# Performance work log

Measured on AMD Instinct MI355X. Metric: run time of the kernel, lower is better.

Reference implementation:

```python
import jax, jax.numpy as jnp
import numpy as np

B, N, S, K = 8, 4096, 2048, 64          # clouds, points/cloud, fps samples (ratio=0.5), max neighbors
C_IN, HID, OUT = 64, 128, 128
RADIUS = 0.2
EPS = 1e-5


def fps(p, s):
    """Farthest point sampling on p:[N,3]; deterministic start at index 0. Returns [s] indices."""
    def step(carry, _):
        min_d, last = carry
        d = jnp.sum((p - p[last]) ** 2, axis=-1)
        min_d = jnp.minimum(min_d, d)
        return (min_d, jnp.argmax(min_d).astype(jnp.int32)), last
    init = (jnp.full((p.shape[0],), jnp.inf, p.dtype), jnp.int32(0))
    _, idx = jax.lax.scan(step, init, None, length=s)
    return idx


def bn_act(h, g, be, mask):
    # masked batch-norm over all valid edges (training-mode stats), then ReLU
    m = mask[..., None].astype(h.dtype)
    cnt = jnp.sum(m)
    mean = jnp.sum(h * m, axis=(0, 1, 2)) / cnt
    var = jnp.sum(((h - mean) ** 2) * m, axis=(0, 1, 2)) / cnt
    return jax.nn.relu((h - mean) * jax.lax.rsqrt(var + EPS) * g + be)


def setup_inputs() -> dict:
    key = jax.random.key(0)
    ks = jax.random.split(key, 8)
    x = jax.random.normal(ks[0], (B * N, C_IN), jnp.float32)
    pos = jax.random.uniform(ks[1], (B * N, 3), jnp.float32)
    batch = jnp.repeat(jnp.arange(B, dtype=jnp.int32), N)
    c0 = C_IN + 3
    W0 = jax.random.normal(ks[2], (c0, HID), jnp.float32) / np.sqrt(c0).astype(np.float32)
    W1 = jax.random.normal(ks[3], (HID, HID), jnp.float32) / np.sqrt(HID).astype(np.float32)
    W2 = jax.random.normal(ks[4], (HID, OUT), jnp.float32) / np.sqrt(HID).astype(np.float32)
    z = lambda n: jnp.zeros((n,), jnp.float32)
    o = lambda n: jnp.ones((n,), jnp.float32)
    return dict(x=x, pos=pos, batch=batch,
                W0=W0, b0=z(HID), g0=o(HID), be0=z(HID),
                W1=W1, b1=z(HID), g1=o(HID), be1=z(HID),
                W2=W2, b2=z(OUT))


def reference(x, pos, batch, W0, b0, g0, be0, W1, b1, g1, be1, W2, b2):
    posb = pos.reshape(B, N, 3)
    xb = x.reshape(B, N, C_IN)
    idx = jax.vmap(lambda p: fps(p, S))(posb)                       # [B,S]
    ctr = jnp.take_along_axis(posb, idx[..., None], axis=1)          # [B,S,3] sampled centroids
    # radius graph: K nearest within RADIUS (mask the rest)
    d2 = jnp.sum((ctr[:, :, None, :] - posb[:, None, :, :]) ** 2, axis=-1)  # [B,S,N]
    negd, nbr = jax.lax.top_k(-d2, K)                                # [B,S,K]
    mask = (-negd) <= RADIUS ** 2
    bix = jnp.arange(B)[:, None, None]
    pos_j = posb[bix, nbr]                                           # [B,S,K,3]
    x_j = xb[bix, nbr]                                               # [B,S,K,C_IN]
    feat = jnp.concatenate([x_j, pos_j - ctr[:, :, None, :]], axis=-1)  # [B,S,K,C_IN+3]
    h = bn_act(feat @ W0 + b0, g0, be0, mask)
    h = bn_act(h @ W1 + b1, g1, be1, mask)
    h = h @ W2 + b2                                                  # plain last layer
    h = jnp.where(mask[..., None], h, -jnp.inf)
    out = jnp.max(h, axis=2)                                         # max aggregation -> [B,S,OUT]
    batch_out = jnp.take_along_axis(batch.reshape(B, N), idx, axis=1).reshape(-1)
    return out.reshape(B * S, OUT), ctr.reshape(B * S, 3), batch_out
```

## Files before the change

### kernel.cpp

```cpp
#include <hip/hip_runtime.h>

typedef _Float16 half8 __attribute__((ext_vector_type(8)));
typedef float floatx4 __attribute__((ext_vector_type(4)));

#define B_   8
#define N_   4096
#define S_   2048
#define K_   64
#define CIN  64
#define HID_ 128
#define Q_   (B_*S_)

#define WS_STATS 0u
#define WS_CNTT  4096u
#define WS_W0T   4224u
#define WS_W1T   28800u
#define WS_W2T   61568u
#define WS_SC0   94336u
#define WS_SH0   94848u
#define WS_SC1   95360u
#define WS_SH1   95872u
#define WS_CNT   96384u
#define WS_NBR   161920u

__global__ __launch_bounds__(256) void k_prep(const float* __restrict__ W0,
        const float* __restrict__ W1, const float* __restrict__ W2,
        _Float16* __restrict__ w0t, _Float16* __restrict__ w1t, _Float16* __restrict__ w2t,
        unsigned long long* __restrict__ stats, int* __restrict__ cntT) {
    int t = blockIdx.x * 256 + threadIdx.x;
    if (t < 128 * 96) {
        int c = t / 96, k = t - c * 96;
        w0t[t] = (k < 67) ? (_Float16)W0[k * 128 + c] : (_Float16)0.f;
    } else if (t < 128 * 96 + 16384) {
        int u = t - 128 * 96; int c = u >> 7, k = u & 127;
        w1t[u] = (_Float16)W1[k * 128 + c];
    } else if (t < 128 * 96 + 32768) {
        int u = t - 128 * 96 - 16384; int c = u >> 7, k = u & 127;
        w2t[u] = (_Float16)W2[k * 128 + c];
    }
    if (t < 512) stats[t] = 0ULL;
    if (t == 0) *cntT = 0;
}

template<int CTRL>
__device__ inline unsigned long long dpp64(unsigned long long v) {
    int lo = (int)(unsigned)v, hi = (int)(unsigned)(v >> 32);
    int nlo = __builtin_amdgcn_update_dpp(lo, lo, CTRL, 0xF, 0xF, false);
    int nhi = __builtin_amdgcn_update_dpp(hi, hi, CTRL, 0xF, 0xF, false);
    return ((unsigned long long)(unsigned)nhi << 32) | (unsigned long long)(unsigned)nlo;
}
__device__ inline unsigned long long u64max(unsigned long long a, unsigned long long b) {
    return (b > a) ? b : a;
}

__global__ __launch_bounds__(256) void k_fps(const float* __restrict__ pos,
        float* __restrict__ outCtr, float* __restrict__ outBatch) {
    __shared__ __align__(16) float4 sP4[N_];
    __shared__ __align__(16) unsigned long long red[2][4];
    __shared__ unsigned short sSeq[S_];
    int b = blockIdx.x, tid = threadIdx.x;
    const float* P = pos + (size_t)b * N_ * 3;

    float px[16], py[16], pz[16], md[16];
    {
        const float4* vp = (const float4*)(P + tid * 48);
        float a[48];
        #pragma unroll
        for (int v = 0; v < 12; v++) {
            float4 t4 = vp[v];
            a[v*4] = t4.x; a[v*4+1] = t4.y; a[v*4+2] = t4.z; a[v*4+3] = t4.w;
        }
        #pragma unroll
        for (int j = 0; j < 16; j++) {
            px[j] = a[3*j]; py[j] = a[3*j+1]; pz[j] = a[3*j+2];
            md[j] = __builtin_inff();
            sP4[tid * 16 + j] = make_float4(px[j], py[j], pz[j], 0.f);
        }
    }
    __syncthreads();

    int last = 0;
    for (int i = 0; i < S_; i++) {
        float4 cc = sP4[last];
        if (tid == (i & 255)) sSeq[i] = (unsigned short)last;
        unsigned long long best;
        {
            #pragma clang fp contract(off)
            float bv = -1.f; unsigned bi = 0;
            #pragma unroll
            for (int j = 0; j < 16; j++) {
                float dx = px[j] - cc.x, dy = py[j] - cc.y, dz = pz[j] - cc.z;
                float d = (dx * dx + dy * dy) + dz * dz;
                float m = fminf(md[j], d); md[j] = m;
                if (m > bv) { bv = m; bi = (unsigned)j; }
            }
            best = ((unsigned long long)__float_as_uint(bv) << 32)
                 | (unsigned long long)(0xFFFFu - (unsigned)(tid * 16) - bi);
        }
        best = u64max(best, dpp64<0x111>(best));
        best = u64max(best, dpp64<0x112>(best));
        best = u64max(best, dpp64<0x114>(best));
        best = u64max(best, dpp64<0x118>(best));
        best = u64max(best, dpp64<0x142>(best));
        best = u64max(best, dpp64<0x143>(best));
        if ((tid & 63) == 63) red[i & 1][tid >> 6] = best;
        __syncthreads();
        ulonglong2 ra = *(const ulonglong2*)&red[i & 1][0];
        ulonglong2 rb = *(const ulonglong2*)&red[i & 1][2];
        unsigned long long g = u64max(u64max(ra.x, ra.y), u64max(rb.x, rb.y));
        last = (int)(0xFFFFu - (unsigned)(g & 0xFFFFu));
    }
    __syncthreads();
    for (int i = tid; i < S_; i += 256) {
        int o = b * S_ + i;
        float4 c = sP4[sSeq[i]];
        outCtr[o*3] = c.x; outCtr[o*3+1] = c.y; outCtr[o*3+2] = c.z;
        outBatch[o] = (float)b;
    }
}

__global__ __launch_bounds__(256) void k_nbr(const float* __restrict__ pos,
        const float* __restrict__ ctr, unsigned short* __restrict__ nbr,
        int* __restrict__ cnt, int* __restrict__ cntT) {
    __shared__ float cD[1024];
    __shared__ unsigned short cI[1024];
    __shared__ int cN;
    int q = blockIdx.x, tid = threadIdx.x;
    int b = q >> 11;
    if (tid == 0) cN = 0;
    __syncthreads();
    float cx = ctr[q*3], cy = ctr[q*3+1], cz = ctr[q*3+2];
    const float* P = pos + (size_t)b * N_ * 3;
    float a[48];
    {
        const float4* vp = (const float4*)(P + (size_t)tid * 48);
        #pragma unroll
        for (int v = 0; v < 12; v++) {
            float4 t4 = vp[v];
            a[v*4] = t4.x; a[v*4+1] = t4.y; a[v*4+2] = t4.z; a[v*4+3] = t4.w;
        }
    }
    unsigned msk = 0;
    float d2a[16];
    {
        #pragma clang fp contract(off)
        #pragma unroll
        for (int j = 0; j < 16; j++) {
            float dx = cx - a[3*j], dy = cy - a[3*j+1], dz = cz - a[3*j+2];
            float d2 = (dx * dx + dy * dy) + dz * dz;
            d2a[j] = d2;
            if (d2 <= 0.04f) msk |= 1u << j;
        }
    }
    int myc = __popc(msk);
    int base = 0;
    if (myc) base = atomicAdd(&cN, myc);
    unsigned mm = msk;
    while (mm) {
        int j = __builtin_ctz(mm); mm &= mm - 1;
        if (base < 1024) { cD[base] = d2a[j]; cI[base] = (unsigned short)(tid * 16 + j); }
        base++;
    }
    __syncthreads();
    int M = min(cN, 1024);
    int V = min(M, K_);
    for (int i = tid; i < M; i += 256) {
        float di = cD[i]; int ii = (int)cI[i]; int r = 0;
        for (int j = 0; j < M; j++) {
            float dj = cD[j];
            r += (dj < di) || (dj == di && (int)cI[j] < ii);
        }
        if (r < K_) nbr[q * K_ + r] = (unsigned short)ii;
    }
    if (tid == 0) { cnt[q] = V; atomicAdd(cntT, V); }
}

__global__ void k_bnparam(const unsigned long long* __restrict__ stats, const int* __restrict__ cntT,
        const float* __restrict__ g, const float* __restrict__ be,
        float* __restrict__ scale, float* __restrict__ shift) {
    int t = threadIdx.x;
    double c = (double)(*cntT);
    double mean = (double)(long long)stats[t] * (1.0 / 1048576.0) / c;
    double ex2  = (double)(long long)stats[128 + t] * (1.0 / 1048576.0) / c;
    double var = ex2 - mean * mean;
    if (var < 0.0) var = 0.0;
    double sc = (double)g[t] / sqrt(var + 1e-5);
    scale[t] = (float)sc;
    shift[t] = (float)((double)be[t] - mean * sc);
}

template<int STAGE>
__global__ __launch_bounds__(256, 2) void k_mlp(const float* __restrict__ x,
        const float* __restrict__ pos, const float* __restrict__ ctr,
        const unsigned short* __restrict__ nbr, const int* __restrict__ cnt,
        const _Float16* __restrict__ w0t, const _Float16* __restrict__ w1t,
        const _Float16* __restrict__ w2t,
        const float* __restrict__ b0, const float* __restrict__ b1,
        const float* __restrict__ b2,
        const float* __restrict__ sc0, const float* __restrict__ sh0,
        const float* __restrict__ sc1, const float* __restrict__ sh1,
        unsigned long long* __restrict__ statsOut, float* __restrict__ outF) {
    __shared__ __align__(16) _Float16 sBuf[64 * 136];
    __shared__ unsigned short sNbr[64];
    __shared__ float sB0v[128];
    __shared__ float sB1v[(STAGE >= 1) ? 128 : 4];
    __shared__ float sSc0[(STAGE >= 1) ? 128 : 4];
    __shared__ float sSh0[(STAGE >= 1) ? 128 : 4];
    __shared__ float sB2v[(STAGE >= 2) ? 128 : 4];
    __shared__ float sSc1[(STAGE >= 2) ? 128 : 4];
    __shared__ float sSh1[(STAGE >= 2) ? 128 : 4];

    int tid = threadIdx.x, wid = tid >> 6, lane = tid & 63;
    int lr = lane & 15, lq = lane >> 4;
    int colbase = 32 * wid + lr;

    half8 w0f[3][2];
    #pragma unroll
    for (int ks = 0; ks < 3; ks++)
        #pragma unroll
        for (int nt = 0; nt < 2; nt++)
            w0f[ks][nt] = *(const half8*)(w0t + (colbase + 16*nt) * 96 + ks * 32 + lq * 8);
    half8 w1f[(STAGE >= 1) ? 4 : 1][2];
    if constexpr (STAGE >= 1)
        #pragma unroll
        for (int ks = 0; ks < 4; ks++)
            #pragma unroll
            for (int nt = 0; nt < 2; nt++)
                w1f[ks][nt] = *(const half8*)(w1t + (colbase + 16*nt) * 128 + ks * 32 + lq * 8);
    half8 w2f[(STAGE >= 2) ? 4 : 1][2];
    if constexpr (STAGE >= 2)
        #pragma unroll
        for (int ks = 0; ks < 4; ks++)
            #pragma unroll
            for (int nt = 0; nt < 2; nt++)
                w2f[ks][nt] = *(const half8*)(w2t + (colbase + 16*nt) * 128 + ks * 32 + lq * 8);

    if (tid < 128) {
        sB0v[tid] = b0[tid];
        if constexpr (STAGE >= 1) { sB1v[tid] = b1[tid]; sSc0[tid] = sc0[tid]; sSh0[tid] = sh0[tid]; }
        if constexpr (STAGE >= 2) { sB2v[tid] = b2[tid]; sSc1[tid] = sc1[tid]; sSh1[tid] = sh1[tid]; }
    }
    float runS1[2] = {0.f, 0.f}, runS2[2] = {0.f, 0.f};

    for (int qq = 0; qq < 8; qq++) {
        int q = blockIdx.x * 8 + qq;
        int b = q >> 11;
        __syncthreads();
        int n = cnt[q];
        if (tid < 64) sNbr[tid] = nbr[q * K_ + tid];
        __syncthreads();
        {
            int row = tid >> 2, c4 = (tid & 3) * 16;
            half8 o0, o1;
            #pragma unroll
            for (int e = 0; e < 8; e++) { o0[e] = (_Float16)0.f; o1[e] = (_Float16)0.f; }
            if (row < n) {
                const float4* xr = (const float4*)(x + ((size_t)b * N_ + sNbr[row]) * CIN + c4);
                float4 v0 = xr[0], v1 = xr[1], v2 = xr[2], v3 = xr[3];
                o0[0]=(_Float16)v0.x; o0[1]=(_Float16)v0.y; o0[2]=(_Float16)v0.z; o0[3]=(_Float16)v0.w;
                o0[4]=(_Float16)v1.x; o0[5]=(_Float16)v1.y; o0[6]=(_Float16)v1.z; o0[7]=(_Float16)v1.w;
                o1[0]=(_Float16)v2.x; o1[1]=(_Float16)v2.y; o1[2]=(_Float16)v2.z; o1[3]=(_Float16)v2.w;
                o1[4]=(_Float16)v3.x; o1[5]=(_Float16)v3.y; o1[6]=(_Float16)v3.z; o1[7]=(_Float16)v3.w;
            }
            *(half8*)&sBuf[row * 104 + c4]     = o0;
            *(half8*)&sBuf[row * 104 + c4 + 8] = o1;
        }
        if (tid < 64) {
            half8 z, o;
            #pragma unroll
            for (int e = 0; e < 8; e++) { z[e] = (_Float16)0.f; o[e] = (_Float16)0.f; }
            if (tid < n) {
                int j = sNbr[tid];
                float cx = ctr[q*3], cy = ctr[q*3+1], cz = ctr[q*3+2];
                const float* pj = pos + ((size_t)b * N_ + j) * 3;
                o[0] = (_Float16)(pj[0] - cx); o[1] = (_Float16)(pj[1] - cy); o[2] = (_Float16)(pj[2] - cz);
            }
            *(half8*)&sBuf[tid * 104 + 64] = o;
            *(half8*)&sBuf[tid * 104 + 72] = z;
            *(half8*)&sBuf[tid * 104 + 80] = z;
            *(half8*)&sBuf[tid * 104 + 88] = z;
        }
        __syncthreads();

        floatx4 acc[4][2];
        #pragma unroll
        for (int rt = 0; rt < 4; rt++)
            #pragma unroll
            for (int nt = 0; nt < 2; nt++)
                #pragma unroll
                for (int r = 0; r < 4; r++) acc[rt][nt][r] = 0.f;
        #pragma unroll
        for (int ks = 0; ks < 3; ks++) {
            half8 av[4];
            #pragma unroll
            for (int rt = 0; rt < 4; rt++)
                av[rt] = *(const half8*)&sBuf[(rt * 16 + lr) * 104 + ks * 32 + lq * 8];
            #pragma unroll
            for (int rt = 0; rt < 4; rt++)
                #pragma unroll
                for (int nt = 0; nt < 2; nt++)
                    acc[rt][nt] = __builtin_amdgcn_mfma_f32_16x16x32_f16(av[rt], w0f[ks][nt], acc[rt][nt], 0, 0, 0);
        }
        __syncthreads();

        if constexpr (STAGE == 0) {
            #pragma unroll
            for (int nt = 0; nt < 2; nt++) {
                int col = colbase + 16 * nt;
                float bias = sB0v[col];
                #pragma unroll
                for (int rt = 0; rt < 4; rt++) {
                    int r0 = rt * 16 + lq * 4;
                    #pragma unroll
                    for (int r = 0; r < 4; r++) {
                        float v = acc[rt][nt][r] + bias;
                        if (r0 + r < n) { runS1[nt] += v; runS2[nt] += v * v; }
                    }
                }
            }
        } else {
            #pragma unroll
            for (int nt = 0; nt < 2; nt++) {
                int col = colbase + 16 * nt;
                float bias = sB0v[col], s = sSc0[col], t2 = sSh0[col];
                #pragma unroll
                for (int rt = 0; rt < 4; rt++) {
                    int r0 = rt * 16 + lq * 4;
                    #pragma unroll
                    for (int r = 0; r < 4; r++) {
                        float v = (acc[rt][nt][r] + bias) * s + t2;
                        sBuf[(r0 + r) * 136 + col] = (_Float16)fmaxf(v, 0.f);
                    }
                }
            }
            __syncthreads();
            #pragma unroll
            for (int rt = 0; rt < 4; rt++)
                #pragma unroll
                for (int nt = 0; nt < 2; nt++)
                    #pragma unroll
                    for (int r = 0; r < 4; r++) acc[rt][nt][r] = 0.f;
            #pragma unroll
            for (int ks = 0; ks < 4; ks++) {
                half8 av[4];
                #pragma unroll
                for (int rt = 0; rt < 4; rt++)
                    av[rt] = *(const half8*)&sBuf[(rt * 16 + lr) * 136 + ks * 32 + lq * 8];
                #pragma unroll
                for (int rt = 0; rt < 4; rt++)
                    #pragma unroll
                    for (int nt = 0; nt < 2; nt++)
                        acc[rt][nt] = __builtin_amdgcn_mfma_f32_16x16x32_f16(av[rt], w1f[ks][nt], acc[rt][nt], 0, 0, 0);
            }

            if constexpr (STAGE == 1) {
                #pragma unroll
                for (int nt = 0; nt < 2; nt++) {
                    int col = colbase + 16 * nt;
                    float bias = sB1v[col];
                    #pragma unroll
                    for (int rt = 0; rt < 4; rt++) {
                        int r0 = rt * 16 + lq * 4;
                        #pragma unroll
                        for (int r = 0; r < 4; r++) {
                            float v = acc[rt][nt][r] + bias;
                            if (r0 + r < n) { runS1[nt] += v; runS2[nt] += v * v; }
                        }
                    }
                }
            } else {
                __syncthreads();
                #pragma unroll
                for (int nt = 0; nt < 2; nt++) {
                    int col = colbase + 16 * nt;
                    float bias = sB1v[col], s = sSc1[col], t2 = sSh1[col];
                    #pragma unroll
                    for (int rt = 0; rt < 4; rt++) {
                        int r0 = rt * 16 + lq * 4;
                        #pragma unroll
                        for (int r = 0; r < 4; r++) {
                            float v = (acc[rt][nt][r] + bias) * s + t2;
                            sBuf[(r0 + r) * 136 + col] = (_Float16)fmaxf(v, 0.f);
                        }
                    }
                }
                __syncthreads();
                #pragma unroll
                for (int rt = 0; rt < 4; rt++)
                    #pragma unroll
                    for (int nt = 0; nt < 2; nt++)
                        #pragma unroll
                        for (int r = 0; r < 4; r++) acc[rt][nt][r] = 0.f;
                #pragma unroll
                for (int ks = 0; ks < 4; ks++) {
                    half8 av[4];
                    #pragma unroll
                    for (int rt = 0; rt < 4; rt++)
                        av[rt] = *(const half8*)&sBuf[(rt * 16 + lr) * 136 + ks * 32 + lq * 8];
                    #pragma unroll
                    for (int rt = 0; rt < 4; rt++)
                        #pragma unroll
                        for (int nt = 0; nt < 2; nt++)
                            acc[rt][nt] = __builtin_amdgcn_mfma_f32_16x16x32_f16(av[rt], w2f[ks][nt], acc[rt][nt], 0, 0, 0);
                }
                #pragma unroll
                for (int nt = 0; nt < 2; nt++) {
                    int col = colbase + 16 * nt;
                    float bias = sB2v[col];
                    float m = -__builtin_inff();
                    #pragma unroll
                    for (int rt = 0; rt < 4; rt++) {
                        int r0 = rt * 16 + lq * 4;
                        #pragma unroll
                        for (int r = 0; r < 4; r++)
                            if (r0 + r < n) m = fmaxf(m, acc[rt][nt][r] + bias);
                    }
                    m = fmaxf(m, __shfl_xor(m, 16));
                    m = fmaxf(m, __shfl_xor(m, 32));
                    if (lq == 0) outF[(size_t)q * 128 + col] = m;
                }
            }
        }
    }
    if constexpr (STAGE <= 1) {
        #pragma unroll
        for (int nt = 0; nt < 2; nt++) {
            float s1 = runS1[nt], s2 = runS2[nt];
            s1 += __shfl_xor(s1, 16); s1 += __shfl_xor(s1, 32);
            s2 += __shfl_xor(s2, 16); s2 += __shfl_xor(s2, 32);
            if (lq == 0) {
                int col = colbase + 16 * nt;
                atomicAdd(&statsOut[col],       (unsigned long long)(long long)llrintf(s1 * 1048576.f));
                atomicAdd(&statsOut[128 + col], (unsigned long long)(long long)llrintf(s2 * 1048576.f));
            }
        }
    }
}

extern "C" void kernel_launch(void* const* d_in, const int* in_sizes, int n_in,
                              void* d_out, int out_size, void* d_ws, size_t ws_size,
                              hipStream_t stream) {
    const float* x   = (const float*)d_in[0];
    const float* pos = (const float*)d_in[1];
    const float* W0  = (const float*)d_in[3];
    const float* b0  = (const float*)d_in[4];
    const float* g0  = (const float*)d_in[5];
    const float* be0 = (const float*)d_in[6];
    const float* W1  = (const float*)d_in[7];
    const float* b1  = (const float*)d_in[8];
    const float* g1  = (const float*)d_in[9];
    const float* be1 = (const float*)d_in[10];
    const float* W2  = (const float*)d_in[11];
    const float* b2  = (const float*)d_in[12];

    char* ws = (char*)d_ws;
    unsigned long long* stats = (unsigned long long*)(ws + WS_STATS);
    int* cntT = (int*)(ws + WS_CNTT);
    _Float16* w0t = (_Float16*)(ws + WS_W0T);
    _Float16* w1t = (_Float16*)(ws + WS_W1T);
    _Float16* w2t = (_Float16*)(ws + WS_W2T);
    float* sc0 = (float*)(ws + WS_SC0);
    float* sh0 = (float*)(ws + WS_SH0);
    float* sc1 = (float*)(ws + WS_SC1);
    float* sh1 = (float*)(ws + WS_SH1);
    int* cnt = (int*)(ws + WS_CNT);
    unsigned short* nbr = (unsigned short*)(ws + WS_NBR);

    float* outF = (float*)d_out;
    float* outCtr = (float*)d_out + 2097152;
    float* outBatch = (float*)d_out + 2146304;

    k_prep<<<176, 256, 0, stream>>>(W0, W1, W2, w0t, w1t, w2t, stats, cntT);
    k_fps<<<B_, 256, 0, stream>>>(pos, outCtr, outBatch);
    k_nbr<<<Q_, 256, 0, stream>>>(pos, outCtr, nbr, cnt, cntT);
    k_mlp<0><<<Q_/8, 256, 0, stream>>>(x, pos, outCtr, nbr, cnt, w0t, w1t, w2t,
            b0, b1, b2, sc0, sh0, sc1, sh1, stats, outF);
    k_bnparam<<<1, 128, 0, stream>>>(stats, cntT, g0, be0, sc0, sh0);
    k_mlp<1><<<Q_/8, 256, 0, stream>>>(x, pos, outCtr, nbr, cnt, w0t, w1t, w2t,
            b0, b1, b2, sc0, sh0, sc1, sh1, stats + 256, outF);
    k_bnparam<<<1, 128, 0, stream>>>(stats + 256, cntT, g1, be1, sc1, sh1);
    k_mlp<2><<<Q_/8, 256, 0, stream>>>(x, pos, outCtr, nbr, cnt, w0t, w1t, w2t,
            b0, b1, b2, sc0, sh0, sc1, sh1, stats, outF);
}
```

Before: 1.956 ms.

## Overlap FPS with neighbor search and layer-0 stats in a persistent front kernel

Merges FPS, radius neighbor search and the first MLP layer's batch-norm statistics into one kernel. Eight blocks run FPS and publish centroids in chunks of 64 through a progress counter with release/acquire atomics. The remaining 248 persistent blocks spin-wait on that counter, then compute neighbors and layer-0 statistics while FPS is still running, so FPS's serial latency is no longer idle time for the rest of the GPU. This relies on all 256 blocks being resident at once, since a waiting consumer must not block the FPS producers. The separate stage-0 MLP pass is removed, and later stages now always recompute layer 0 with the BN applied.

```diff
diff --git a/kernel.cpp b/kernel.cpp
--- a/kernel.cpp
+++ b/kernel.cpp
@@ -10,6 +10,7 @@
 #define CIN  64
 #define HID_ 128
 #define Q_   (B_*S_)
+#define NCONS 248
 
 #define WS_STATS 0u
 #define WS_CNTT  4096u
@@ -22,11 +23,12 @@
 #define WS_SH1   95872u
 #define WS_CNT   96384u
 #define WS_NBR   161920u
+#define WS_PROG  2259072u
 
 __global__ __launch_bounds__(256) void k_prep(const float* __restrict__ W0,
         const float* __restrict__ W1, const float* __restrict__ W2,
         _Float16* __restrict__ w0t, _Float16* __restrict__ w1t, _Float16* __restrict__ w2t,
-        unsigned long long* __restrict__ stats, int* __restrict__ cntT) {
+        unsigned long long* __restrict__ stats, int* __restrict__ cntT, int* __restrict__ prog) {
     int t = blockIdx.x * 256 + threadIdx.x;
     if (t < 128 * 96) {
         int c = t / 96, k = t - c * 96;
@@ -39,6 +41,7 @@
         w2t[u] = (_Float16)W2[k * 128 + c];
     }
     if (t < 512) stats[t] = 0ULL;
+    if (t < 8) prog[t] = 0;
     if (t == 0) *cntT = 0;
 }
 
@@ -53,126 +56,239 @@
     return (b > a) ? b : a;
 }
 
-__global__ __launch_bounds__(256) void k_fps(const float* __restrict__ pos,
-        float* __restrict__ outCtr, float* __restrict__ outBatch) {
-    __shared__ __align__(16) float4 sP4[N_];
-    __shared__ __align__(16) unsigned long long red[2][4];
-    __shared__ unsigned short sSeq[S_];
-    int b = blockIdx.x, tid = threadIdx.x;
-    const float* P = pos + (size_t)b * N_ * 3;
-
-    float px[16], py[16], pz[16], md[16];
-    {
-        const float4* vp = (const float4*)(P + tid * 48);
-        float a[48];
-        #pragma unroll
-        for (int v = 0; v < 12; v++) {
-            float4 t4 = vp[v];
-            a[v*4] = t4.x; a[v*4+1] = t4.y; a[v*4+2] = t4.z; a[v*4+3] = t4.w;
-        }
-        #pragma unroll
-        for (int j = 0; j < 16; j++) {
-            px[j] = a[3*j]; py[j] = a[3*j+1]; pz[j] = a[3*j+2];
-            md[j] = __builtin_inff();
-            sP4[tid * 16 + j] = make_float4(px[j], py[j], pz[j], 0.f);
+__global__ __launch_bounds__(256) void k_front(const float* __restrict__ pos,
+        const float* __restrict__ x, const _Float16* __restrict__ w0t,
+        const float* __restrict__ b0, float* outCtr, float* __restrict__ outBatch,
+        unsigned short* __restrict__ nbrG, int* __restrict__ cnt, int* __restrict__ cntT,
+        unsigned long long* __restrict__ statsOut, int* prog) {
+    __shared__ __align__(16) char uLDS[69760];
+    int tid = threadIdx.x;
+
+    if (blockIdx.x < 8) {
+        float4* sP4 = (float4*)uLDS;
+        unsigned long long* red = (unsigned long long*)(uLDS + 65536);
+        unsigned short* sSeq = (unsigned short*)(uLDS + 65600);
+        int b = blockIdx.x;
+        const float* P = pos + (size_t)b * N_ * 3;
+
+        float px[16], py[16], pz[16], md[16];
+        {
+            const float4* vp = (const float4*)(P + tid * 48);
+            float a[48];
+            #pragma unroll
+            for (int v = 0; v < 12; v++) {
+                float4 t4 = vp[v];
+                a[v*4] = t4.x; a[v*4+1] = t4.y; a[v*4+2] = t4.z; a[v*4+3] = t4.w;
+            }
+            #pragma unroll
+            for (int j = 0; j < 16; j++) {
+                px[j] = a[3*j]; py[j] = a[3*j+1]; pz[j] = a[3*j+2];
+                md[j] = __builtin_inff();
+                sP4[tid * 16 + j] = make_float4(px[j], py[j], pz[j], 0.f);
+            }
+        }
+        __syncthreads();
+
+        int last = 0;
+        for (int i = 0; i < S_; i++) {
+            float4 cc = sP4[last];
+            if (tid == (i & 255)) sSeq[i] = (unsigned short)last;
+            unsigned long long best;
+            {
+                #pragma clang fp contract(off)
+                float bv = -1.f; unsigned bi = 0;
+                #pragma unroll
+                for (int j = 0; j < 16; j++) {
+                    float dx = px[j] - cc.x, dy = py[j] - cc.y, dz = pz[j] - cc.z;
+                    float d = (dx * dx + dy * dy) + dz * dz;
+                    float m = fminf(md[j], d); md[j] = m;
+                    if (m > bv) { bv = m; bi = (unsigned)j; }
+                }
+                best = ((unsigned long long)__float_as_uint(bv) << 32)
+                     | (unsigned long long)(0xFFFFu - (unsigned)(tid * 16) - bi);
+            }
+            best = u64max(best, dpp64<0x111>(best));
+            best = u64max(best, dpp64<0x112>(best));
+            best = u64max(best, dpp64<0x114>(best));
+            best = u64max(best, dpp64<0x118>(best));
+            best = u64max(best, dpp64<0x142>(best));
+            best = u64max(best, dpp64<0x143>(best));
+            if ((tid & 63) == 63) red[(i & 1) * 4 + (tid >> 6)] = best;
+            __syncthreads();
+            ulonglong2 ra = *(const ulonglong2*)&red[(i & 1) * 4];
+            ulonglong2 rb = *(const ulonglong2*)&red[(i & 1) * 4 + 2];
+            unsigned long long g = u64max(u64max(ra.x, ra.y), u64max(rb.x, rb.y));
+            last = (int)(0xFFFFu - (unsigned)(g & 0xFFFFu));
+            if ((i & 63) == 63) {
+                if (tid < 64) {
+                    int ii = i - 63 + tid;
+                    float4 c = sP4[sSeq[ii]];
+                    size_t o = (size_t)b * S_ + ii;
+                    __hip_atomic_store(&outCtr[o*3],   c.x, __ATOMIC_RELAXED, __HIP_MEMORY_SCOPE_AGENT);
+                    __hip_atomic_store(&outCtr[o*3+1], c.y, __ATOMIC_RELAXED, __HIP_MEMORY_SCOPE_AGENT);
+                    __hip_atomic_store(&outCtr[o*3+2], c.z, __ATOMIC_RELAXED, __HIP_MEMORY_SCOPE_AGENT);
+                    outBatch[o] = (float)b;
+                }
+                __syncthreads();
+                if (tid == 0)
+                    __hip_atomic_store(&prog[b], i + 1, __ATOMIC_RELEASE, __HIP_MEMORY_SCOPE_AGENT);
+            }
+        }
+    } else {
+        float* cD = (float*)uLDS;
+        unsigned short* cI = (unsigned short*)(uLDS + 4096);
+        unsigned short* sNbr = (unsigned short*)(uLDS + 6144);
+        float* sB0v = (float*)(uLDS + 6272);
+        float* sCtr = (float*)(uLDS + 6784);
+        int* cN = (int*)(uLDS + 6800);
+        _Float16* sBuf = (_Float16*)(uLDS + 6912);
+
+        int wid = tid >> 6, lane = tid & 63;
+        int lr = lane & 15, lq = lane >> 4;
+        int colbase = 32 * wid + lr;
+        half8 w0f[3][2];
+        #pragma unroll
+        for (int ks = 0; ks < 3; ks++)
+            #pragma unroll
+            for (int nt = 0; nt < 2; nt++)
+                w0f[ks][nt] = *(const half8*)(w0t + (colbase + 16*nt) * 96 + ks * 32 + lq * 8);
+        if (tid < 128) sB0v[tid] = b0[tid];
+        float runS1[2] = {0.f, 0.f}, runS2[2] = {0.f, 0.f};
+
+        for (int k = (int)blockIdx.x - 8; k < Q_; k += NCONS) {
+            int i = k >> 3, b = k & 7;
+            int q = (b << 11) + i;
+            if (tid == 0) {
+                while (__hip_atomic_load(&prog[b], __ATOMIC_ACQUIRE, __HIP_MEMORY_SCOPE_AGENT) <= i)
+                    __builtin_amdgcn_s_sleep(32);
+                sCtr[0] = __hip_atomic_load(&outCtr[(size_t)q*3],   __ATOMIC_RELAXED, __HIP_MEMORY_SCOPE_AGENT);
+                sCtr[1] = __hip_atomic_load(&outCtr[(size_t)q*3+1], __ATOMIC_RELAXED, __HIP_MEMORY_SCOPE_AGENT);
+                sCtr[2] = __hip_atomic_load(&outCtr[(size_t)q*3+2], __ATOMIC_RELAXED, __HIP_MEMORY_SCOPE_AGENT);
+                *cN = 0;
+            }
+            __syncthreads();
+            float cx = sCtr[0], cy = sCtr[1], cz = sCtr[2];
+            const float* P = pos + (size_t)b * N_ * 3;
+            float a[48];
+            {
+                const float4* vp = (const float4*)(P + (size_t)tid * 48);
+                #pragma unroll
+                for (int v = 0; v < 12; v++) {
+                    float4 t4 = vp[v];
+                    a[v*4] = t4.x; a[v*4+1] = t4.y; a[v*4+2] = t4.z; a[v*4+3] = t4.w;
+                }
+            }
+            unsigned msk = 0;
+            float d2a[16];
+            {
+                #pragma clang fp contract(off)
+                #pragma unroll
+                for (int j = 0; j < 16; j++) {
+                    float dx = cx - a[3*j], dy = cy - a[3*j+1], dz = cz - a[3*j+2];
+                    float d2 = (dx * dx + dy * dy) + dz * dz;
+                    d2a[j] = d2;
+                    if (d2 <= 0.04f) msk |= 1u << j;
+                }
+            }
+            int myc = __popc(msk);
+            int base = 0;
+            if (myc) base = atomicAdd(cN, myc);
+            unsigned mm = msk;
+            while (mm) {
+                int j = __builtin_ctz(mm); mm &= mm - 1;
+                if (base < 1024) { cD[base] = d2a[j]; cI[base] = (unsigned short)(tid * 16 + j); }
+                base++;
+            }
+            __syncthreads();
+            int M = min(*cN, 1024);
+            int n = min(M, K_);
+            for (int i2 = tid; i2 < M; i2 += 256) {
+                float di = cD[i2]; int ii = (int)cI[i2]; int r = 0;
+                for (int j = 0; j < M; j++) {
+                    float dj = cD[j];
+                    r += (dj < di) || (dj == di && (int)cI[j] < ii);
+                }
+                if (r < K_) { nbrG[q * K_ + r] = (unsigned short)ii; sNbr[r] = (unsigned short)ii; }
+            }
+            if (tid == 0) { cnt[q] = n; atomicAdd(cntT, n); }
+            __syncthreads();
+            {
+                int row = tid >> 2, c4 = (tid & 3) * 16;
+                half8 o0, o1;
+                #pragma unroll
+                for (int e = 0; e < 8; e++) { o0[e] = (_Float16)0.f; o1[e] = (_Float16)0.f; }
+                if (row < n) {
+                    const float4* xr = (const float4*)(x + ((size_t)b * N_ + sNbr[row]) * CIN + c4);
+                    float4 v0 = xr[0], v1 = xr[1], v2 = xr[2], v3 = xr[3];
+                    o0[0]=(_Float16)v0.x; o0[1]=(_Float16)v0.y; o0[2]=(_Float16)v0.z; o0[3]=(_Float16)v0.w;
+                    o0[4]=(_Float16)v1.x; o0[5]=(_Float16)v1.y; o0[6]=(_Float16)v1.z; o0[7]=(_Float16)v1.w;
+                    o1[0]=(_Float16)v2.x; o1[1]=(_Float16)v2.y; o1[2]=(_Float16)v2.z; o1[3]=(_Float16)v2.w;
+                    o1[4]=(_Float16)v3.x; o1[5]=(_Float16)v3.y; o1[6]=(_Float16)v3.z; o1[7]=(_Float16)v3.w;
+                }
+                *(half8*)&sBuf[row * 104 + c4]     = o0;
+                *(half8*)&sBuf[row * 104 + c4 + 8] = o1;
+            }
+            if (tid < 64) {
+                half8 z, o;
+                #pragma unroll
+                for (int e = 0; e < 8; e++) { z[e] = (_Float16)0.f; o[e] = (_Float16)0.f; }
+                if (tid < n) {
+                    int j = sNbr[tid];
+                    const float* pj = pos + ((size_t)b * N_ + j) * 3;
+                    o[0] = (_Float16)(pj[0] - cx); o[1] = (_Float16)(pj[1] - cy); o[2] = (_Float16)(pj[2] - cz);
+                }
+                *(half8*)&sBuf[tid * 104 + 64] = o;
+                *(half8*)&sBuf[tid * 104 + 72] = z;
+                *(half8*)&sBuf[tid * 104 + 80] = z;
+                *(half8*)&sBuf[tid * 104 + 88] = z;
+            }
+            __syncthreads();
+            floatx4 acc[4][2];
+            #pragma unroll
+            for (int rt = 0; rt < 4; rt++)
+                #pragma unroll
+                for (int nt = 0; nt < 2; nt++)
+                    #pragma unroll
+                    for (int r = 0; r < 4; r++) acc[rt][nt][r] = 0.f;
+            #pragma unroll
+            for (int ks = 0; ks < 3; ks++) {
+                half8 av[4];
+                #pragma unroll
+                for (int rt = 0; rt < 4; rt++)
+                    av[rt] = *(const half8*)&sBuf[(rt * 16 + lr) * 104 + ks * 32 + lq * 8];
+                #pragma unroll
+                for (int rt = 0; rt < 4; rt++)
+                    #pragma unroll
+                    for (int nt = 0; nt < 2; nt++)
+                        acc[rt][nt] = __builtin_amdgcn_mfma_f32_16x16x32_f16(av[rt], w0f[ks][nt], acc[rt][nt], 0, 0, 0);
+            }
+            #pragma unroll
+            for (int nt = 0; nt < 2; nt++) {
+                int col = colbase + 16 * nt;
+                float bias = sB0v[col];
+                #pragma unroll
+                for (int rt = 0; rt < 4; rt++) {
+                    int r0 = rt * 16 + lq * 4;
+                    #pragma unroll
+                    for (int r = 0; r < 4; r++) {
+                        float v = acc[rt][nt][r] + bias;
+                        if (r0 + r < n) { runS1[nt] += v; runS2[nt] += v * v; }
+                    }
+                }
+            }
+        }
+        #pragma unroll
+        for (int nt = 0; nt < 2; nt++) {
+            float s1 = runS1[nt], s2 = runS2[nt];
+            s1 += __shfl_xor(s1, 16); s1 += __shfl_xor(s1, 32);
+            s2 += __shfl_xor(s2, 16); s2 += __shfl_xor(s2, 32);
+            if (lq == 0) {
+                int col = colbase + 16 * nt;
+                atomicAdd(&statsOut[col],       (unsigned long long)(long long)llrintf(s1 * 1048576.f));
+                atomicAdd(&statsOut[128 + col], (unsigned long long)(long long)llrintf(s2 * 1048576.f));
+            }
         }
     }
-    __syncthreads();
-
-    int last = 0;
-    for (int i = 0; i < S_; i++) {
-        float4 cc = sP4[last];
-        if (tid == (i & 255)) sSeq[i] = (unsigned short)last;
-        unsigned long long best;
-        {
-            #pragma clang fp contract(off)
-            float bv = -1.f; unsigned bi = 0;
-            #pragma unroll
-            for (int j = 0; j < 16; j++) {
-                float dx = px[j] - cc.x, dy = py[j] - cc.y, dz = pz[j] - cc.z;
-                float d = (dx * dx + dy * dy) + dz * dz;
-                float m = fminf(md[j], d); md[j] = m;
-                if (m > bv) { bv = m; bi = (unsigned)j; }
-            }
-            best = ((unsigned long long)__float_as_uint(bv) << 32)
-                 | (unsigned long long)(0xFFFFu - (unsigned)(tid * 16) - bi);
-        }
-        best = u64max(best, dpp64<0x111>(best));
-        best = u64max(best, dpp64<0x112>(best));
-        best = u64max(best, dpp64<0x114>(best));
-        best = u64max(best, dpp64<0x118>(best));
-        best = u64max(best, dpp64<0x142>(best));
-        best = u64max(best, dpp64<0x143>(best));
-        if ((tid & 63) == 63) red[i & 1][tid >> 6] = best;
-        __syncthreads();
-        ulonglong2 ra = *(const ulonglong2*)&red[i & 1][0];
-        ulonglong2 rb = *(const ulonglong2*)&red[i & 1][2];
-        unsigned long long g = u64max(u64max(ra.x, ra.y), u64max(rb.x, rb.y));
-        last = (int)(0xFFFFu - (unsigned)(g & 0xFFFFu));
-    }
-    __syncthreads();
-    for (int i = tid; i < S_; i += 256) {
-        int o = b * S_ + i;
-        float4 c = sP4[sSeq[i]];
-        outCtr[o*3] = c.x; outCtr[o*3+1] = c.y; outCtr[o*3+2] = c.z;
-        outBatch[o] = (float)b;
-    }
-}
-
-__global__ __launch_bounds__(256) void k_nbr(const float* __restrict__ pos,
-        const float* __restrict__ ctr, unsigned short* __restrict__ nbr,
-        int* __restrict__ cnt, int* __restrict__ cntT) {
-    __shared__ float cD[1024];
-    __shared__ unsigned short cI[1024];
-    __shared__ int cN;
-    int q = blockIdx.x, tid = threadIdx.x;
-    int b = q >> 11;
-    if (tid == 0) cN = 0;
-    __syncthreads();
-    float cx = ctr[q*3], cy = ctr[q*3+1], cz = ctr[q*3+2];
-    const float* P = pos + (size_t)b * N_ * 3;
-    float a[48];
-    {
-        const float4* vp = (const float4*)(P + (size_t)tid * 48);
-        #pragma unroll
-        for (int v = 0; v < 12; v++) {
-            float4 t4 = vp[v];
-            a[v*4] = t4.x; a[v*4+1] = t4.y; a[v*4+2] = t4.z; a[v*4+3] = t4.w;
-        }
-    }
-    unsigned msk = 0;
-    float d2a[16];
-    {
-        #pragma clang fp contract(off)
-        #pragma unroll
-        for (int j = 0; j < 16; j++) {
-            float dx = cx - a[3*j], dy = cy - a[3*j+1], dz = cz - a[3*j+2];
-            float d2 = (dx * dx + dy * dy) + dz * dz;
-            d2a[j] = d2;
-            if (d2 <= 0.04f) msk |= 1u << j;
-        }
-    }
-    int myc = __popc(msk);
-    int base = 0;
-    if (myc) base = atomicAdd(&cN, myc);
-    unsigned mm = msk;
-    while (mm) {
-        int j = __builtin_ctz(mm); mm &= mm - 1;
-        if (base < 1024) { cD[base] = d2a[j]; cI[base] = (unsigned short)(tid * 16 + j); }
-        base++;
-    }
-    __syncthreads();
-    int M = min(cN, 1024);
-    int V = min(M, K_);
-    for (int i = tid; i < M; i += 256) {
-        float di = cD[i]; int ii = (int)cI[i]; int r = 0;
-        for (int j = 0; j < M; j++) {
-            float dj = cD[j];
-            r += (dj < di) || (dj == di && (int)cI[j] < ii);
-        }
-        if (r < K_) nbr[q * K_ + r] = (unsigned short)ii;
-    }
-    if (tid == 0) { cnt[q] = V; atomicAdd(cntT, V); }
 }
 
 __global__ void k_bnparam(const unsigned long long* __restrict__ stats, const int* __restrict__ cntT,
@@ -203,9 +319,9 @@
     __shared__ __align__(16) _Float16 sBuf[64 * 136];
     __shared__ unsigned short sNbr[64];
     __shared__ float sB0v[128];
-    __shared__ float sB1v[(STAGE >= 1) ? 128 : 4];
-    __shared__ float sSc0[(STAGE >= 1) ? 128 : 4];
-    __shared__ float sSh0[(STAGE >= 1) ? 128 : 4];
+    __shared__ float sB1v[128];
+    __shared__ float sSc0[128];
+    __shared__ float sSh0[128];
     __shared__ float sB2v[(STAGE >= 2) ? 128 : 4];
     __shared__ float sSc1[(STAGE >= 2) ? 128 : 4];
     __shared__ float sSh1[(STAGE >= 2) ? 128 : 4];
@@ -220,13 +336,12 @@
         #pragma unroll
         for (int nt = 0; nt < 2; nt++)
             w0f[ks][nt] = *(const half8*)(w0t + (colbase + 16*nt) * 96 + ks * 32 + lq * 8);
-    half8 w1f[(STAGE >= 1) ? 4 : 1][2];
-    if constexpr (STAGE >= 1)
-        #pragma unroll
-        for (int ks = 0; ks < 4; ks++)
-            #pragma unroll
-            for (int nt = 0; nt < 2; nt++)
-                w1f[ks][nt] = *(const half8*)(w1t + (colbase + 16*nt) * 128 + ks * 32 + lq * 8);
+    half8 w1f[4][2];
+    #pragma unroll
+    for (int ks = 0; ks < 4; ks++)
+        #pragma unroll
+        for (int nt = 0; nt < 2; nt++)
+            w1f[ks][nt] = *(const half8*)(w1t + (colbase + 16*nt) * 128 + ks * 32 + lq * 8);
     half8 w2f[(STAGE >= 2) ? 4 : 1][2];
     if constexpr (STAGE >= 2)
         #pragma unroll
@@ -237,7 +352,7 @@
 
     if (tid < 128) {
         sB0v[tid] = b0[tid];
-        if constexpr (STAGE >= 1) { sB1v[tid] = b1[tid]; sSc0[tid] = sc0[tid]; sSh0[tid] = sh0[tid]; }
+        sB1v[tid] = b1[tid]; sSc0[tid] = sc0[tid]; sSh0[tid] = sh0[tid];
         if constexpr (STAGE >= 2) { sB2v[tid] = b2[tid]; sSc1[tid] = sc1[tid]; sSh1[tid] = sh1[tid]; }
     }
     float runS1[2] = {0.f, 0.f}, runS2[2] = {0.f, 0.f};
@@ -303,11 +418,45 @@
         }
         __syncthreads();
 
-        if constexpr (STAGE == 0) {
+        #pragma unroll
+        for (int nt = 0; nt < 2; nt++) {
+            int col = colbase + 16 * nt;
+            float bias = sB0v[col], s = sSc0[col], t2 = sSh0[col];
+            #pragma unroll
+            for (int rt = 0; rt < 4; rt++) {
+                int r0 = rt * 16 + lq * 4;
+                #pragma unroll
+                for (int r = 0; r < 4; r++) {
+                    float v = (acc[rt][nt][r] + bias) * s + t2;
+                    sBuf[(r0 + r) * 136 + col] = (_Float16)fmaxf(v, 0.f);
+                }
+            }
+        }
+        __syncthreads();
+        #pragma unroll
+        for (int rt = 0; rt < 4; rt++)
+            #pragma unroll
+            for (int nt = 0; nt < 2; nt++)
+                #pragma unroll
+                for (int r = 0; r < 4; r++) acc[rt][nt][r] = 0.f;
+        #pragma unroll
+        for (int ks = 0; ks < 4; ks++) {
+            half8 av[4];
+            #pragma unroll
+            for (int rt = 0; rt < 4; rt++)
+                av[rt] = *(const half8*)&sBuf[(rt * 16 + lr) * 136 + ks * 32 + lq * 8];
+            #pragma unroll
+            for (int rt = 0; rt < 4; rt++)
+                #pragma unroll
+                for (int nt = 0; nt < 2; nt++)
+                    acc[rt][nt] = __builtin_amdgcn_mfma_f32_16x16x32_f16(av[rt], w1f[ks][nt], acc[rt][nt], 0, 0, 0);
+        }
+
+        if constexpr (STAGE == 1) {
             #pragma unroll
             for (int nt = 0; nt < 2; nt++) {
                 int col = colbase + 16 * nt;
-                float bias = sB0v[col];
+                float bias = sB1v[col];
                 #pragma unroll
                 for (int rt = 0; rt < 4; rt++) {
                     int r0 = rt * 16 + lq * 4;
@@ -319,10 +468,11 @@
                 }
             }
         } else {
+            __syncthreads();
             #pragma unroll
             for (int nt = 0; nt < 2; nt++) {
                 int col = colbase + 16 * nt;
-                float bias = sB0v[col], s = sSc0[col], t2 = sSh0[col];
+                float bias = sB1v[col], s = sSc1[col], t2 = sSh1[col];
                 #pragma unroll
                 for (int rt = 0; rt < 4; rt++) {
                     int r0 = rt * 16 + lq * 4;
@@ -350,79 +500,27 @@
                 for (int rt = 0; rt < 4; rt++)
                     #pragma unroll
                     for (int nt = 0; nt < 2; nt++)
-                        acc[rt][nt] = __builtin_amdgcn_mfma_f32_16x16x32_f16(av[rt], w1f[ks][nt], acc[rt][nt], 0, 0, 0);
-            }
-
-            if constexpr (STAGE == 1) {
-                #pragma unroll
-                for (int nt = 0; nt < 2; nt++) {
-                    int col = colbase + 16 * nt;
-                    float bias = sB1v[col];
-                    #pragma unroll
-                    for (int rt = 0; rt < 4; rt++) {
-                        int r0 = rt * 16 + lq * 4;
-                        #pragma unroll
-                        for (int r = 0; r < 4; r++) {
-                            float v = acc[rt][nt][r] + bias;
-                            if (r0 + r < n) { runS1[nt] += v; runS2[nt] += v * v; }
-                        }
-                    }
-                }
-            } else {
-                __syncthreads();
-                #pragma unroll
-                for (int nt = 0; nt < 2; nt++) {
-                    int col = colbase + 16 * nt;
-                    float bias = sB1v[col], s = sSc1[col], t2 = sSh1[col];
-                    #pragma unroll
-                    for (int rt = 0; rt < 4; rt++) {
-                        int r0 = rt * 16 + lq * 4;
-                        #pragma unroll
-                        for (int r = 0; r < 4; r++) {
-                            float v = (acc[rt][nt][r] + bias) * s + t2;
-                            sBuf[(r0 + r) * 136 + col] = (_Float16)fmaxf(v, 0.f);
-                        }
-                    }
-                }
-                __syncthreads();
-                #pragma unroll
-                for (int rt = 0; rt < 4; rt++)
-                    #pragma unroll
-                    for (int nt = 0; nt < 2; nt++)
-                        #pragma unroll
-                        for (int r = 0; r < 4; r++) acc[rt][nt][r] = 0.f;
-                #pragma unroll
-                for (int ks = 0; ks < 4; ks++) {
-                    half8 av[4];
-                    #pragma unroll
-                    for (int rt = 0; rt < 4; rt++)
-                        av[rt] = *(const half8*)&sBuf[(rt * 16 + lr) * 136 + ks * 32 + lq * 8];
-                    #pragma unroll
-                    for (int rt = 0; rt < 4; rt++)
-                        #pragma unroll
-                        for (int nt = 0; nt < 2; nt++)
-                            acc[rt][nt] = __builtin_amdgcn_mfma_f32_16x16x32_f16(av[rt], w2f[ks][nt], acc[rt][nt], 0, 0, 0);
-                }
-                #pragma unroll
-                for (int nt = 0; nt < 2; nt++) {
-                    int col = colbase + 16 * nt;
-                    float bias = sB2v[col];
-                    float m = -__builtin_inff();
-                    #pragma unroll
-                    for (int rt = 0; rt < 4; rt++) {
-                        int r0 = rt * 16 + lq * 4;
-                        #pragma unroll
-                        for (int r = 0; r < 4; r++)
-                            if (r0 + r < n) m = fmaxf(m, acc[rt][nt][r] + bias);
-                    }
-                    m = fmaxf(m, __shfl_xor(m, 16));
-                    m = fmaxf(m, __shfl_xor(m, 32));
-                    if (lq == 0) outF[(size_t)q * 128 + col] = m;
-                }
+                        acc[rt][nt] = __builtin_amdgcn_mfma_f32_16x16x32_f16(av[rt], w2f[ks][nt], acc[rt][nt], 0, 0, 0);
+            }
+            #pragma unroll
+            for (int nt = 0; nt < 2; nt++) {
+                int col = colbase + 16 * nt;
+                float bias = sB2v[col];
+                float m = -__builtin_inff();
+                #pragma unroll
+                for (int rt = 0; rt < 4; rt++) {
+                    int r0 = rt * 16 + lq * 4;
+                    #pragma unroll
+                    for (int r = 0; r < 4; r++)
+                        if (r0 + r < n) m = fmaxf(m, acc[rt][nt][r] + bias);
+                }
+                m = fmaxf(m, __shfl_xor(m, 16));
+                m = fmaxf(m, __shfl_xor(m, 32));
+                if (lq == 0) outF[(size_t)q * 128 + col] = m;
             }
         }
     }
-    if constexpr (STAGE <= 1) {
+    if constexpr (STAGE == 1) {
         #pragma unroll
         for (int nt = 0; nt < 2; nt++) {
             float s1 = runS1[nt], s2 = runS2[nt];
@@ -465,16 +563,15 @@
     float* sh1 = (float*)(ws + WS_SH1);
     int* cnt = (int*)(ws + WS_CNT);
     unsigned short* nbr = (unsigned short*)(ws + WS_NBR);
+    int* prog = (int*)(ws + WS_PROG);
 
     float* outF = (float*)d_out;
     float* outCtr = (float*)d_out + 2097152;
     float* outBatch = (float*)d_out + 2146304;
 
-    k_prep<<<176, 256, 0, stream>>>(W0, W1, W2, w0t, w1t, w2t, stats, cntT);
-    k_fps<<<B_, 256, 0, stream>>>(pos, outCtr, outBatch);
-    k_nbr<<<Q_, 256, 0, stream>>>(pos, outCtr, nbr, cnt, cntT);
-    k_mlp<0><<<Q_/8, 256, 0, stream>>>(x, pos, outCtr, nbr, cnt, w0t, w1t, w2t,
-            b0, b1, b2, sc0, sh0, sc1, sh1, stats, outF);
+    k_prep<<<176, 256, 0, stream>>>(W0, W1, W2, w0t, w1t, w2t, stats, cntT, prog);
+    k_front<<<256, 256, 0, stream>>>(pos, x, w0t, b0, outCtr, outBatch, nbr, cnt, cntT,
+            stats, prog);
     k_bnparam<<<1, 128, 0, stream>>>(stats, cntT, g0, be0, sc0, sh0);
     k_mlp<1><<<Q_/8, 256, 0, stream>>>(x, pos, outCtr, nbr, cnt, w0t, w1t, w2t,
             b0, b1, b2, sc0, sh0, sc1, sh1, stats + 256, outF);
```

New measurement: 1.743 ms. 1.12x faster.
